# Performance work log

Measured on AMD Instinct MI355X. Metric: run time of the kernel, lower is better.

## Reference

```python
import jax, jax.numpy as jnp
import numpy as np

B, LQ, D, H, L, P, DFF = 16, 1024, 256, 8, 4, 4, 1024
SHAPES = ((64, 64), (32, 32), (16, 16), (8, 8))  # (H_l, W_l) per level
LV = sum(h * w for h, w in SHAPES)  # 5440
DH = D // H
EPS = 1e-5


def layer_norm(x, g, b):
    m = jnp.mean(x, -1, keepdims=True)
    v = jnp.mean((x - m) ** 2, -1, keepdims=True)
    return (x - m) * jax.lax.rsqrt(v + EPS) * g + b


def mha(q_in, k_in, v_in, w, b, ow, ob):
    # torch nn.MultiheadAttention with packed in_proj [3D, D]
    q = (q_in @ w[:D].T + b[:D]).reshape(B, LQ, H, DH)
    k = (k_in @ w[D:2 * D].T + b[D:2 * D]).reshape(B, LQ, H, DH)
    v = (v_in @ w[2 * D:].T + b[2 * D:]).reshape(B, LQ, H, DH)
    a = jax.nn.softmax(jnp.einsum('bqhd,bkhd->bhqk', q, k) * (1.0 / np.sqrt(DH)), -1)
    o = jnp.einsum('bhqk,bkhd->bqhd', a, v).reshape(B, LQ, D)
    return o @ ow.T + ob


def ms_deform_attn(q, ref, src, value_w, value_b, off_w, off_b, attw_w, attw_b, outp_w, outp_b):
    # value: [B, H, LV, DH]
    value = (src @ value_w.T + value_b).reshape(B, LV, H, DH).transpose(0, 2, 1, 3)
    off = (q @ off_w.T + off_b).reshape(B, LQ, H, L, P, 2)
    attw = jax.nn.softmax((q @ attw_w.T + attw_b).reshape(B, LQ, H, L * P), -1).reshape(B, LQ, H, L, P)
    # offset normalizer = (W_l, H_l) matching (x, y) order of reference points
    normalizer = jnp.array([[w, h] for h, w in SHAPES], jnp.float32)
    loc = ref[:, :, None, :, None, :] + off / normalizer[None, None, None, :, None, :]  # [B,LQ,H,L,P,2]
    out = jnp.zeros((B, LQ, H, DH), jnp.float32)
    start = 0
    for l, (hl, wl) in enumerate(SHAPES):
        v = value[:, :, start:start + hl * wl]  # [B,H,N_l,DH]
        start += hl * wl
        # grid_sample semantics, align_corners=False, padding zeros
        x = loc[:, :, :, l, :, 0] * wl - 0.5  # [B,LQ,H,P]
        y = loc[:, :, :, l, :, 1] * hl - 0.5
        x0 = jnp.floor(x); y0 = jnp.floor(y)
        lx = (x - x0).transpose(0, 2, 1, 3)[..., None]  # [B,H,LQ,P,1]
        ly = (y - y0).transpose(0, 2, 1, 3)[..., None]
        x0i = x0.astype(jnp.int32); y0i = y0.astype(jnp.int32)

        def gather(xi, yi):
            valid = ((xi >= 0) & (xi < wl) & (yi >= 0) & (yi < hl)).astype(jnp.float32)
            idx = jnp.clip(yi, 0, hl - 1) * wl + jnp.clip(xi, 0, wl - 1)  # [B,LQ,H,P]
            idx2 = idx.transpose(0, 2, 1, 3).reshape(B, H, LQ * P)
            g = jnp.take_along_axis(v, jnp.broadcast_to(idx2[..., None], (B, H, LQ * P, DH)), axis=2)
            return g.reshape(B, H, LQ, P, DH) * valid.transpose(0, 2, 1, 3)[..., None]

        g00 = gather(x0i, y0i); g01 = gather(x0i + 1, y0i)
        g10 = gather(x0i, y0i + 1); g11 = gather(x0i + 1, y0i + 1)
        sampled = (g00 * (1 - lx) * (1 - ly) + g01 * lx * (1 - ly)
                   + g10 * (1 - lx) * ly + g11 * lx * ly)  # [B,H,LQ,P,DH]
        out = out + jnp.einsum('bhqpd,bqhp->bqhd', sampled, attw[:, :, :, l])
    return out.reshape(B, LQ, D) @ outp_w.T + outp_b


def setup_inputs() -> dict:
    key = jax.random.key(0)
    ks = jax.random.split(key, 16)
    s = 0.02
    inp = {}
    inp['tgt'] = jax.random.normal(ks[0], (B, LQ, D), jnp.float32)
    inp['query_pos'] = jax.random.normal(ks[1], (B, LQ, D), jnp.float32)
    inp['reference_points'] = jax.random.uniform(ks[2], (B, LQ, L, 2), jnp.float32)
    inp['src'] = jax.random.normal(ks[3], (B, LV, D), jnp.float32)
    # self-attention (MHA)
    inp['in_proj_w'] = jax.random.normal(ks[4], (3 * D, D), jnp.float32) * s
    inp['in_proj_b'] = jnp.zeros((3 * D,), jnp.float32)
    inp['out_proj_w'] = jax.random.normal(ks[5], (D, D), jnp.float32) * s
    inp['out_proj_b'] = jnp.zeros((D,), jnp.float32)
    inp['norm2_g'] = jnp.ones((D,), jnp.float32); inp['norm2_b'] = jnp.zeros((D,), jnp.float32)
    # MSDeformAttn
    inp['value_w'] = jax.random.normal(ks[6], (D, D), jnp.float32) * s
    inp['value_b'] = jnp.zeros((D,), jnp.float32)
    inp['off_w'] = jax.random.normal(ks[7], (H * L * P * 2, D), jnp.float32) * s
    inp['off_b'] = jax.random.normal(ks[8], (H * L * P * 2,), jnp.float32) * 0.5
    inp['attw_w'] = jax.random.normal(ks[9], (H * L * P, D), jnp.float32) * s
    inp['attw_b'] = jnp.zeros((H * L * P,), jnp.float32)
    inp['outp_w'] = jax.random.normal(ks[10], (D, D), jnp.float32) * s
    inp['outp_b'] = jnp.zeros((D,), jnp.float32)
    inp['norm1_g'] = jnp.ones((D,), jnp.float32); inp['norm1_b'] = jnp.zeros((D,), jnp.float32)
    # FFN
    inp['lin1_w'] = jax.random.normal(ks[11], (DFF, D), jnp.float32) * s
    inp['lin1_b'] = jnp.zeros((DFF,), jnp.float32)
    inp['lin2_w'] = jax.random.normal(ks[12], (D, DFF), jnp.float32) * s
    inp['lin2_b'] = jnp.zeros((D,), jnp.float32)
    inp['norm3_g'] = jnp.ones((D,), jnp.float32); inp['norm3_b'] = jnp.zeros((D,), jnp.float32)
    inp['src_spatial_shapes'] = jnp.array(SHAPES, jnp.int32)
    inp['level_start_index'] = jnp.array(np.concatenate([[0], np.cumsum([h * w for h, w in SHAPES[:-1]])]), jnp.int32)
    return inp


def reference(tgt, query_pos, reference_points, src,
              in_proj_w, in_proj_b, out_proj_w, out_proj_b, norm2_g, norm2_b,
              value_w, value_b, off_w, off_b, attw_w, attw_b, outp_w, outp_b,
              norm1_g, norm1_b, lin1_w, lin1_b, lin2_w, lin2_b, norm3_g, norm3_b,
              src_spatial_shapes, level_start_index):
    # dropout=0 (eval mode)
    q = tgt + query_pos
    tgt2 = mha(q, q, tgt, in_proj_w, in_proj_b, out_proj_w, out_proj_b)
    tgt = layer_norm(tgt + tgt2, norm2_g, norm2_b)
    tgt2 = ms_deform_attn(tgt + query_pos, reference_points, src,
                          value_w, value_b, off_w, off_b, attw_w, attw_b, outp_w, outp_b)
    tgt = layer_norm(tgt + tgt2, norm1_g, norm1_b)
    t2 = jax.nn.relu(tgt @ lin1_w.T + lin1_b) @ lin2_w.T + lin2_b
    return layer_norm(tgt + t2, norm3_g, norm3_b)
```

## Files before the change

### kernel.cpp

```cpp
#include <hip/hip_runtime.h>
#include <math.h>

typedef short s16x8 __attribute__((ext_vector_type(8)));
typedef float f32x4 __attribute__((ext_vector_type(4)));
typedef unsigned short u16;
typedef unsigned short u16x4 __attribute__((ext_vector_type(4)));

constexpr int cB    = 16;
constexpr int cLQ   = 1024;
constexpr int cD    = 256;
constexpr int cH    = 8;
constexpr int cLVTOT= 5440;
constexpr int cNTOK = cB * cLQ;
constexpr int cNV   = cB * cLVTOT;

__device__ __forceinline__ u16 f2b(float f) {
    __bf16 h = (__bf16)f;
    u16 u;
    __builtin_memcpy(&u, &h, 2);
    return u;
}
__device__ __forceinline__ float bl(unsigned x) {
    return __uint_as_float(x << 16);
}
__device__ __forceinline__ void load16(const u16* g, u16* l) {
    __builtin_amdgcn_global_load_lds((const __attribute__((address_space(1))) void*)g,
                                     (__attribute__((address_space(3))) void*)l, 16, 0, 0);
}

__global__ __launch_bounds__(256) void cvt_kernel(const float4* __restrict__ in,
                                                  u16x4* __restrict__ out) {
    int i = blockIdx.x * 256 + threadIdx.x;
    float4 v = in[i];
    out[i] = (u16x4){ f2b(v.x), f2b(v.y), f2b(v.z), f2b(v.w) };
}

struct WArgs { const float4* src[8]; };
__global__ __launch_bounds__(256) void cvtw_kernel(WArgs a, u16x4* __restrict__ out) {
    int i = blockIdx.x * 256 + threadIdx.x;
    int s, off;
    if (i < 98304) {
        if (i < 65536) { if (i < 49152) { s = 0; off = i; } else { s = 1; off = i - 49152; } }
        else           { if (i < 81920) { s = 2; off = i - 65536; } else { s = 3; off = i - 81920; } }
    } else {
        if (i < 122880){ if (i < 106496){ s = 4; off = i - 98304; } else { s = 5; off = i - 106496; } }
        else           { if (i < 188416){ s = 6; off = i - 122880; } else { s = 7; off = i - 188416; } }
    }
    float4 v = a.src[s][off];
    out[i] = (u16x4){ f2b(v.x), f2b(v.y), f2b(v.z), f2b(v.w) };
}

__global__ __launch_bounds__(256) void prep_kernel(const float4* __restrict__ t,
                                                   const float4* __restrict__ q,
                                                   u16x4* __restrict__ tb,
                                                   u16x4* __restrict__ qb) {
    int i = blockIdx.x * 256 + threadIdx.x;
    float4 a = t[i], b = q[i];
    tb[i] = (u16x4){ f2b(a.x), f2b(a.y), f2b(a.z), f2b(a.w) };
    qb[i] = (u16x4){ f2b(a.x + b.x), f2b(a.y + b.y), f2b(a.z + b.z), f2b(a.w + b.w) };
}

__global__ __launch_bounds__(256) void gemm_qkv(const u16* __restrict__ A0,
                                                const u16* __restrict__ A1,
                                                const u16* __restrict__ Wt,
                                                const float* __restrict__ bias,
                                                u16* __restrict__ QKb,
                                                u16* __restrict__ Vtg) {
    __shared__ u16 As[2][128 * 32];
    __shared__ u16 Bs[2][128 * 32];
    const int K = 256;
    int tid = threadIdx.x;
    int bm = blockIdx.x * 128, bn = blockIdx.y * 128;
    const u16* A = (blockIdx.y < 4) ? A0 : A1;
    int w = tid >> 6, lane = tid & 63, quad = lane >> 4, l15 = lane & 15;
    int wm = (w & 1) * 64, wn = (w >> 1) * 64;
    int r0 = tid >> 2;
    int c0 = ((tid & 3) ^ ((tid >> 3) & 3)) * 8;
    const u16* ga0 = A  + (size_t)(bm + r0) * K + c0;
    const u16* ga1 = ga0 + (size_t)64 * K;
    const u16* gb0 = Wt + (size_t)(bn + r0) * K + c0;
    const u16* gb1 = gb0 + (size_t)64 * K;
    int lofs = (tid & 192) * 8;
    int abk = (quad ^ ((l15 >> 1) & 3)) * 8;
    f32x4 acc[16];
#pragma unroll
    for (int i = 0; i < 16; ++i) acc[i] = (f32x4){0.f, 0.f, 0.f, 0.f};
    load16(ga0, &As[0][lofs]);
    load16(ga1, &As[0][2048 + lofs]);
    load16(gb0, &Bs[0][lofs]);
    load16(gb1, &Bs[0][2048 + lofs]);
#pragma unroll 2
    for (int i = 0; i < 8; ++i) {
        int cur = i & 1, nxt = cur ^ 1;
        int k1 = (i + 1) << 5;
        if (i < 7) {
            load16(ga0 + k1, &As[nxt][lofs]);
            load16(ga1 + k1, &As[nxt][2048 + lofs]);
            load16(gb0 + k1, &Bs[nxt][lofs]);
            load16(gb1 + k1, &Bs[nxt][2048 + lofs]);
        }
        __syncthreads();
        s16x8 af[4], bf[4];
#pragma unroll
        for (int mt = 0; mt < 4; ++mt) af[mt] = *(const s16x8*)&As[cur][(wm + mt * 16 + l15) * 32 + abk];
#pragma unroll
        for (int nt = 0; nt < 4; ++nt) bf[nt] = *(const s16x8*)&Bs[cur][(wn + nt * 16 + l15) * 32 + abk];
#pragma unroll
        for (int mt = 0; mt < 4; ++mt)
#pragma unroll
            for (int nt = 0; nt < 4; ++nt)
                acc[mt * 4 + nt] = __builtin_amdgcn_mfma_f32_16x16x32_bf16(af[mt], bf[nt], acc[mt * 4 + nt], 0, 0, 0);
        __syncthreads();
    }
    float bs[4];
#pragma unroll
    for (int nt = 0; nt < 4; ++nt) bs[nt] = bias[bn + wn + nt * 16 + l15];
    if (bn < 512) {
#pragma unroll
        for (int mt = 0; mt < 4; ++mt) {
            int m = bm + wm + mt * 16 + quad * 4;
#pragma unroll
            for (int nt = 0; nt < 4; ++nt) {
                int n = bn + wn + nt * 16 + l15;
#pragma unroll
                for (int r = 0; r < 4; ++r)
                    QKb[(size_t)(m + r) * 512 + n] = f2b(acc[mt * 4 + nt][r] + bs[nt]);
            }
        }
    } else {
#pragma unroll
        for (int mt = 0; mt < 4; ++mt) {
            int m = bm + wm + mt * 16 + quad * 4;
            int b = m >> 10, t = m & 1023;
#pragma unroll
            for (int nt = 0; nt < 4; ++nt) {
                int nv = bn + wn + nt * 16 + l15 - 512;
                int h = nv >> 5, dh = nv & 31;
                u16x4 o;
#pragma unroll
                for (int r = 0; r < 4; ++r) o[r] = f2b(acc[mt * 4 + nt][r] + bs[nt]);
                *(u16x4*)(Vtg + (((size_t)(b * 8 + h) * 32 + dh) << 10) + t) = o;
            }
        }
    }
}

template <int RELU, int OUTBF>
__global__ __launch_bounds__(256) void gemm128(const u16* __restrict__ A,
                                               const u16* __restrict__ Wt,
                                               const float* __restrict__ bias,
                                               float* __restrict__ Cf,
                                               u16* __restrict__ Cb,
                                               int M, int N, int K) {
    __shared__ u16 As[2][128 * 32];
    __shared__ u16 Bs[2][128 * 32];
    int tid = threadIdx.x;
    int bm = blockIdx.x * 128, bn = blockIdx.y * 128;
    int w = tid >> 6, lane = tid & 63, quad = lane >> 4, l15 = lane & 15;
    int wm = (w & 1) * 64, wn = (w >> 1) * 64;
    int r0 = tid >> 2;
    int c0 = ((tid & 3) ^ ((tid >> 3) & 3)) * 8;
    const u16* ga0 = A  + (size_t)(bm + r0) * K + c0;
    const u16* ga1 = ga0 + (size_t)64 * K;
    const u16* gb0 = Wt + (size_t)(bn + r0) * K + c0;
    const u16* gb1 = gb0 + (size_t)64 * K;
    int lofs = (tid & 192) * 8;
    int abk = (quad ^ ((l15 >> 1) & 3)) * 8;
    f32x4 acc[16];
#pragma unroll
    for (int i = 0; i < 16; ++i) acc[i] = (f32x4){0.f, 0.f, 0.f, 0.f};
    load16(ga0, &As[0][lofs]);
    load16(ga1, &As[0][2048 + lofs]);
    load16(gb0, &Bs[0][lofs]);
    load16(gb1, &Bs[0][2048 + lofs]);
    int nk = K >> 5;
#pragma unroll 2
    for (int i = 0; i < nk; ++i) {
        int cur = i & 1, nxt = cur ^ 1;
        int k1 = (i + 1) << 5;
        if (i + 1 < nk) {
            load16(ga0 + k1, &As[nxt][lofs]);
            load16(ga1 + k1, &As[nxt][2048 + lofs]);
            load16(gb0 + k1, &Bs[nxt][lofs]);
            load16(gb1 + k1, &Bs[nxt][2048 + lofs]);
        }
        __syncthreads();
        s16x8 af[4], bf[4];
#pragma unroll
        for (int mt = 0; mt < 4; ++mt) af[mt] = *(const s16x8*)&As[cur][(wm + mt * 16 + l15) * 32 + abk];
#pragma unroll
        for (int nt = 0; nt < 4; ++nt) bf[nt] = *(const s16x8*)&Bs[cur][(wn + nt * 16 + l15) * 32 + abk];
#pragma unroll
        for (int mt = 0; mt < 4; ++mt)
#pragma unroll
            for (int nt = 0; nt < 4; ++nt)
                acc[mt * 4 + nt] = __builtin_amdgcn_mfma_f32_16x16x32_bf16(af[mt], bf[nt], acc[mt * 4 + nt], 0, 0, 0);
        __syncthreads();
    }
    float bs[4];
#pragma unroll
    for (int nt = 0; nt < 4; ++nt) bs[nt] = bias[bn + wn + nt * 16 + l15];
#pragma unroll
    for (int mt = 0; mt < 4; ++mt) {
        int m = bm + wm + mt * 16 + quad * 4;
#pragma unroll
        for (int nt = 0; nt < 4; ++nt) {
            int n = bn + wn + nt * 16 + l15;
#pragma unroll
            for (int r = 0; r < 4; ++r) {
                float v = acc[mt * 4 + nt][r] + bs[nt];
                if (RELU) v = fmaxf(v, 0.f);
                if (OUTBF) Cb[(size_t)(m + r) * N + n] = f2b(v);
                else       Cf[(size_t)(m + r) * N + n] = v;
            }
        }
    }
}

template <int RELU, int OUTBF>
__global__ __launch_bounds__(256) void gemm64(const u16* __restrict__ A,
                                              const u16* __restrict__ Wt,
                                              const float* __restrict__ bias,
                                              float* __restrict__ Cf,
                                              u16* __restrict__ Cb,
                                              int M, int N, int K) {
    __shared__ u16 As[2][64 * 32];
    __shared__ u16 Bs[2][128 * 32];
    int tid = threadIdx.x;
    int bm = blockIdx.x * 64, bn = blockIdx.y * 128;
    int w = tid >> 6, lane = tid & 63, quad = lane >> 4, l15 = lane & 15;
    int wn = w * 32;
    int r0 = tid >> 2;
    int c0 = ((tid & 3) ^ ((tid >> 3) & 3)) * 8;
    const u16* ga0 = A  + (size_t)(bm + r0) * K + c0;
    const u16* gb0 = Wt + (size_t)(bn + r0) * K + c0;
    const u16* gb1 = gb0 + (size_t)64 * K;
    int lofs = (tid & 192) * 8;
    int abk = (quad ^ ((l15 >> 1) & 3)) * 8;
    f32x4 acc[8];
#pragma unroll
    for (int i = 0; i < 8; ++i) acc[i] = (f32x4){0.f, 0.f, 0.f, 0.f};
    load16(ga0, &As[0][lofs]);
    load16(gb0, &Bs[0][lofs]);
    load16(gb1, &Bs[0][2048 + lofs]);
    int nk = K >> 5;
#pragma unroll 2
    for (int i = 0; i < nk; ++i) {
        int cur = i & 1, nxt = cur ^ 1;
        int k1 = (i + 1) << 5;
        if (i + 1 < nk) {
            load16(ga0 + k1, &As[nxt][lofs]);
            load16(gb0 + k1, &Bs[nxt][lofs]);
            load16(gb1 + k1, &Bs[nxt][2048 + lofs]);
        }
        __syncthreads();
        s16x8 af[4], bf[2];
#pragma unroll
        for (int mt = 0; mt < 4; ++mt) af[mt] = *(const s16x8*)&As[cur][(mt * 16 + l15) * 32 + abk];
#pragma unroll
        for (int nt = 0; nt < 2; ++nt) bf[nt] = *(const s16x8*)&Bs[cur][(wn + nt * 16 + l15) * 32 + abk];
#pragma unroll
        for (int mt = 0; mt < 4; ++mt)
#pragma unroll
            for (int nt = 0; nt < 2; ++nt)
                acc[mt * 2 + nt] = __builtin_amdgcn_mfma_f32_16x16x32_bf16(af[mt], bf[nt], acc[mt * 2 + nt], 0, 0, 0);
        __syncthreads();
    }
    float bs[2];
#pragma unroll
    for (int nt = 0; nt < 2; ++nt) bs[nt] = bias[bn + wn + nt * 16 + l15];
#pragma unroll
    for (int mt = 0; mt < 4; ++mt) {
        int m = bm + mt * 16 + quad * 4;
#pragma unroll
        for (int nt = 0; nt < 2; ++nt) {
            int n = bn + wn + nt * 16 + l15;
#pragma unroll
            for (int r = 0; r < 4; ++r) {
                float v = acc[mt * 2 + nt][r] + bs[nt];
                if (RELU) v = fmaxf(v, 0.f);
                if (OUTBF) Cb[(size_t)(m + r) * N + n] = f2b(v);
                else       Cf[(size_t)(m + r) * N + n] = v;
            }
        }
    }
}

__global__ __launch_bounds__(256) void attn_mfma(const u16* __restrict__ QK,
                                                 const u16* __restrict__ Vt,
                                                 u16* __restrict__ O) {
    __shared__ u16 Ks[64 * 40];
    __shared__ u16 Vs[32 * 72];
    __shared__ u16 Ps[4][16 * 72];
    int tid = threadIdx.x, w = tid >> 6, lane = tid & 63, quad = lane >> 4, l15 = lane & 15;
    int qt = blockIdx.x & 15, bh = blockIdx.x >> 4;
    int h = bh & 7, b = bh >> 3;
    int qbase = qt * 64 + w * 16;
    const float C = 0.25506734f;
    s16x8 qf = *(const s16x8*)(QK + (size_t)(b * cLQ + qbase + l15) * 512 + h * 32 + quad * 8);
    f32x4 o0 = {0.f,0.f,0.f,0.f}, o1 = {0.f,0.f,0.f,0.f};
    float lsum = 0.f;
    int skey = tid >> 2, sdh = (tid & 3) * 8;
    int vdh = tid >> 3, vkc = (tid & 7) * 8;
    size_t kgbase = (size_t)(b * cLQ) * 512 + 256 + h * 32;
    size_t vgbase = (size_t)bh * 32 * cLQ;
    s16x8 kreg = *(const s16x8*)(QK + kgbase + (size_t)skey * 512 + sdh);
    s16x8 vreg = *(const s16x8*)(Vt + vgbase + (size_t)vdh * cLQ + vkc);
    for (int kt = 0; kt < cLQ; kt += 64) {
        __syncthreads();
        *(s16x8*)&Ks[skey * 40 + sdh] = kreg;
        *(s16x8*)&Vs[vdh * 72 + vkc]  = vreg;
        if (kt + 64 < cLQ) {
            kreg = *(const s16x8*)(QK + kgbase + (size_t)(kt + 64 + skey) * 512 + sdh);
            vreg = *(const s16x8*)(Vt + vgbase + (size_t)vdh * cLQ + kt + 64 + vkc);
        }
        __syncthreads();
#pragma unroll
        for (int t = 0; t < 4; ++t) {
            s16x8 kf = *(const s16x8*)&Ks[(t * 16 + l15) * 40 + quad * 8];
            f32x4 z = {0.f,0.f,0.f,0.f};
            f32x4 sc = __builtin_amdgcn_mfma_f32_16x16x32_bf16(kf, qf, z, 0, 0, 0);
            u16x4 pb;
#pragma unroll
            for (int r = 0; r < 4; ++r) {
                float p = exp2f(sc[r] * C);
                lsum += p;
                pb[r] = f2b(p);
            }
            *(u16x4*)&Ps[w][l15 * 72 + t * 16 + quad * 4] = pb;
        }
#pragma unroll
        for (int ks = 0; ks < 2; ++ks) {
            s16x8 pa  = *(const s16x8*)&Ps[w][l15 * 72 + ks * 32 + quad * 8];
            s16x8 vb0 = *(const s16x8*)&Vs[l15 * 72 + ks * 32 + quad * 8];
            s16x8 vb1 = *(const s16x8*)&Vs[(l15 + 16) * 72 + ks * 32 + quad * 8];
            o0 = __builtin_amdgcn_mfma_f32_16x16x32_bf16(pa, vb0, o0, 0, 0, 0);
            o1 = __builtin_amdgcn_mfma_f32_16x16x32_bf16(pa, vb1, o1, 0, 0, 0);
        }
    }
    lsum += __shfl_xor(lsum, 16);
    lsum += __shfl_xor(lsum, 32);
#pragma unroll
    for (int r = 0; r < 4; ++r) {
        float inv = 1.0f / __shfl(lsum, quad * 4 + r);
        int q = qbase + quad * 4 + r;
        size_t ob = (size_t)(b * cLQ + q) * cD + h * 32;
        O[ob + l15]      = f2b(o0[r] * inv);
        O[ob + 16 + l15] = f2b(o1[r] * inv);
    }
}

template <int WB, int QP>
__global__ __launch_bounds__(256) void add_ln_kernel(const float* __restrict__ X,
                                                     const float* __restrict__ R,
                                                     const float* __restrict__ g,
                                                     const float* __restrict__ bt,
                                                     const float* __restrict__ qp,
                                                     float* __restrict__ out,
                                                     u16* __restrict__ outb) {
    int wave = threadIdx.x / 64;
    int lane = threadIdx.x % 64;
    int row = blockIdx.x * 4 + wave;
    const float* x = X + (size_t)row * cD;
    const float* r = R + (size_t)row * cD;
    float4 xv = *(const float4*)(x + lane * 4);
    float4 rv = *(const float4*)(r + lane * 4);
    float v0 = xv.x + rv.x, v1 = xv.y + rv.y, v2 = xv.z + rv.z, v3 = xv.w + rv.w;
    float s = v0 + v1 + v2 + v3;
    float s2 = v0 * v0 + v1 * v1 + v2 * v2 + v3 * v3;
#pragma unroll
    for (int off = 32; off > 0; off >>= 1) {
        s += __shfl_xor(s, off);
        s2 += __shfl_xor(s2, off);
    }
    float mean = s * (1.0f / 256.0f);
    float var = s2 * (1.0f / 256.0f) - mean * mean;
    float rstd = rsqrtf(var + 1e-5f);
    float4 gv = *(const float4*)(g + lane * 4);
    float4 bv = *(const float4*)(bt + lane * 4);
    float4 o;
    o.x = (v0 - mean) * rstd * gv.x + bv.x;
    o.y = (v1 - mean) * rstd * gv.y + bv.y;
    o.z = (v2 - mean) * rstd * gv.z + bv.z;
    o.w = (v3 - mean) * rstd * gv.w + bv.w;
    *(float4*)(out + (size_t)row * cD + lane * 4) = o;
    if (WB) {
        u16x4 ob = { f2b(o.x), f2b(o.y), f2b(o.z), f2b(o.w) };
        *(u16x4*)(outb + (size_t)row * cD + lane * 4) = ob;
    }
    if (QP) {
        float4 qv = *(const float4*)(qp + (size_t)row * cD + lane * 4);
        u16x4 ob = { f2b(o.x + qv.x), f2b(o.y + qv.y), f2b(o.z + qv.z), f2b(o.w + qv.w) };
        *(u16x4*)(outb + (size_t)row * cD + lane * 4) = ob;
    }
}

__global__ __launch_bounds__(256) void deform_kernel(const u16* __restrict__ value,
                                                     const float* __restrict__ oa,
                                                     const float* __restrict__ refp,
                                                     u16* __restrict__ out) {
    int t = blockIdx.x * 32 + (threadIdx.x >> 3);
    int dq = threadIdx.x & 7;
    int h = t & 7;
    int bq = t >> 3;
    int b = bq >> 10;
    const float* al = oa + (size_t)bq * 384 + 256 + h * 16;
    float wv[16];
    float mx = -1e30f;
#pragma unroll
    for (int i = 0; i < 16; ++i) { wv[i] = al[i]; mx = fmaxf(mx, wv[i]); }
    float sum = 0.f;
#pragma unroll
    for (int i = 0; i < 16; ++i) { wv[i] = __expf(wv[i] - mx); sum += wv[i]; }
    float inv = 1.f / sum;
    const float* off = oa + (size_t)bq * 384 + h * 32;
    const float* rp = refp + (size_t)bq * 8;
    const u16* vb = value + ((size_t)b * cLVTOT) * 256 + h * 32 + dq * 4;
    const int starts[4] = {0, 4096, 5120, 5376};
    const int dims[4] = {64, 32, 16, 8};
    float a0 = 0.f, a1 = 0.f, a2 = 0.f, a3 = 0.f;
#pragma unroll
    for (int l = 0; l < 4; ++l) {
        int hl = dims[l], wl = dims[l];
        float rx = rp[l * 2 + 0], ry = rp[l * 2 + 1];
#pragma unroll
        for (int p = 0; p < 4; ++p) {
            float ox = off[(l * 4 + p) * 2 + 0];
            float oy = off[(l * 4 + p) * 2 + 1];
            float x = rx * (float)wl + ox - 0.5f;
            float y = ry * (float)hl + oy - 0.5f;
            float x0f = floorf(x), y0f = floorf(y);
            float lx = x - x0f, ly = y - y0f;
            int x0 = (int)x0f, y0 = (int)y0f;
            float aw = wv[l * 4 + p] * inv;
            float cw[4] = {(1.f - lx) * (1.f - ly), lx * (1.f - ly),
                           (1.f - lx) * ly, lx * ly};
            int xs[4] = {x0, x0 + 1, x0, x0 + 1};
            int ys[4] = {y0, y0, y0 + 1, y0 + 1};
#pragma unroll
            for (int c = 0; c < 4; ++c) {
                int xi = xs[c], yi = ys[c];
                bool valid = (xi >= 0) && (xi < wl) && (yi >= 0) && (yi < hl);
                int xc = min(max(xi, 0), wl - 1);
                int yc = min(max(yi, 0), hl - 1);
                int idx = starts[l] + yc * wl + xc;
                float wgt = valid ? aw * cw[c] : 0.f;
                unsigned long long u = *(const unsigned long long*)(vb + (size_t)idx * 256);
                a0 += wgt * bl((unsigned)(u & 0xffffull));
                a1 += wgt * bl((unsigned)((u >> 16) & 0xffffull));
                a2 += wgt * bl((unsigned)((u >> 32) & 0xffffull));
                a3 += wgt * bl((unsigned)(u >> 48));
            }
        }
    }
    u16x4 o = { f2b(a0), f2b(a1), f2b(a2), f2b(a3) };
    *(u16x4*)(out + (size_t)bq * 256 + h * 32 + dq * 4) = o;
}

extern "C" void kernel_launch(void* const* d_in, const int* in_sizes, int n_in,
                              void* d_out, int out_size, void* d_ws, size_t ws_size,
                              hipStream_t stream) {
    const float* tgt        = (const float*)d_in[0];
    const float* query_pos  = (const float*)d_in[1];
    const float* refp       = (const float*)d_in[2];
    const float* src        = (const float*)d_in[3];
    const float* in_proj_w  = (const float*)d_in[4];
    const float* in_proj_b  = (const float*)d_in[5];
    const float* out_proj_w = (const float*)d_in[6];
    const float* out_proj_b = (const float*)d_in[7];
    const float* norm2_g    = (const float*)d_in[8];
    const float* norm2_b    = (const float*)d_in[9];
    const float* value_w    = (const float*)d_in[10];
    const float* value_b    = (const float*)d_in[11];
    const float* off_b      = (const float*)d_in[13];
    const float* attw_b     = (const float*)d_in[15];
    const float* outp_b     = (const float*)d_in[17];
    const float* norm1_g    = (const float*)d_in[18];
    const float* norm1_b    = (const float*)d_in[19];
    const float* lin1_b     = (const float*)d_in[21];
    const float* lin2_b     = (const float*)d_in[23];
    const float* norm3_g    = (const float*)d_in[24];
    const float* norm3_b    = (const float*)d_in[25];

    char* W = (char*)d_ws;
    const size_t S84 = 8388608;
    u16*   tgtb  = (u16*)(W + 0);
    u16*   q2b   = (u16*)(W + 0);
    u16*   qb    = (u16*)(W + 1 * S84);
    u16*   QKb   = (u16*)(W + 2 * S84);
    u16*   dtb   = (u16*)(W + 2 * S84);
    u16*   x2b   = (u16*)(W + 3 * S84);
    float* ffn2f = (float*)(W + 4 * S84);
    u16*   aob   = (u16*)(W + 5 * S84);
    float* oaf   = (float*)(W + 5 * S84);
    u16*   Vtg   = (u16*)(W + 6 * S84);
    float* t2f   = (float*)(W + 6 * S84);
    float* x1f   = (float*)(W + 8 * S84);
    float* x2f   = (float*)(W + 10 * S84);
    u16*   srcb  = (u16*)(W + 12 * S84);
    u16*   ffn1b = (u16*)(W + 12 * S84);
    u16*   valb  = (u16*)(W + 12 * S84 + 44564480);
    char*  wbase = W + 12 * S84 + 2 * 44564480;
    u16* wb_in   = (u16*)(wbase + 0);
    u16* wb_out  = (u16*)(wbase + 393216);
    u16* wb_val  = (u16*)(wbase + 524288);
    u16* wb_off  = (u16*)(wbase + 655360);
    u16* wb_outp = (u16*)(wbase + 851968);
    u16* wb_lin1 = (u16*)(wbase + 983040);
    u16* wb_lin2 = (u16*)(wbase + 1507328);
    float* biasoa= (float*)(wbase + 2031616);
    float* out = (float*)d_out;

    dim3 blk(256);

    hipMemcpyAsync(biasoa,       off_b,  256 * 4, hipMemcpyDeviceToDevice, stream);
    hipMemcpyAsync(biasoa + 256, attw_b, 128 * 4, hipMemcpyDeviceToDevice, stream);

    prep_kernel<<<dim3(4096), blk, 0, stream>>>((const float4*)tgt, (const float4*)query_pos,
                                                (u16x4*)tgtb, (u16x4*)qb);
    WArgs wa;
    wa.src[0] = (const float4*)in_proj_w;  wa.src[1] = (const float4*)out_proj_w;
    wa.src[2] = (const float4*)value_w;    wa.src[3] = (const float4*)d_in[12];
    wa.src[4] = (const float4*)d_in[14];   wa.src[5] = (const float4*)d_in[16];
    wa.src[6] = (const float4*)d_in[20];   wa.src[7] = (const float4*)d_in[22];
    cvtw_kernel<<<dim3(992), blk, 0, stream>>>(wa, (u16x4*)wb_in);
    cvt_kernel<<<dim3(21760), blk, 0, stream>>>((const float4*)src, (u16x4*)srcb);

    gemm_qkv<<<dim3(128, 6), blk, 0, stream>>>(qb, tgtb, wb_in, in_proj_b, QKb, Vtg);
    attn_mfma<<<dim3(cB * cH * 16), blk, 0, stream>>>(QKb, Vtg, aob);
    gemm64<0, 0><<<dim3(256, 2), blk, 0, stream>>>(aob, wb_out, out_proj_b, t2f, nullptr, cNTOK, 256, 256);
    add_ln_kernel<0, 1><<<dim3(4096), blk, 0, stream>>>(tgt, t2f, norm2_g, norm2_b, query_pos, x1f, q2b);

    gemm128<0, 1><<<dim3(680, 2), blk, 0, stream>>>(srcb, wb_val, value_b, nullptr, valb, cNV, 256, 256);
    gemm64<0, 0><<<dim3(256, 3), blk, 0, stream>>>(q2b, wb_off, biasoa, oaf, nullptr, cNTOK, 384, 256);
    deform_kernel<<<dim3(4096), blk, 0, stream>>>(valb, oaf, refp, dtb);
    gemm64<0, 0><<<dim3(256, 2), blk, 0, stream>>>(dtb, wb_outp, outp_b, t2f, nullptr, cNTOK, 256, 256);
    add_ln_kernel<1, 0><<<dim3(4096), blk, 0, stream>>>(x1f, t2f, norm1_g, norm1_b, nullptr, x2f, x2b);

    gemm128<1, 1><<<dim3(128, 8), blk, 0, stream>>>(x2b, wb_lin1, lin1_b, nullptr, ffn1b, cNTOK, 1024, 256);
    gemm64<0, 0><<<dim3(256, 2), blk, 0, stream>>>(ffn1b, wb_lin2, lin2_b, ffn2f, nullptr, cNTOK, 256, 1024);
    add_ln_kernel<0, 0><<<dim3(4096), blk, 0, stream>>>(x2f, ffn2f, norm3_g, norm3_b, nullptr, out, nullptr);
}
```

Before: 458.0 us.

## Stage GEMM tiles through registers, fuse prep kernels, fold softmax scale into Q

```diff
diff --git a/kernel.cpp b/kernel.cpp
--- a/kernel.cpp
+++ b/kernel.cpp
@@ -23,21 +23,38 @@
 __device__ __forceinline__ float bl(unsigned x) {
     return __uint_as_float(x << 16);
 }
-__device__ __forceinline__ void load16(const u16* g, u16* l) {
-    __builtin_amdgcn_global_load_lds((const __attribute__((address_space(1))) void*)g,
-                                     (__attribute__((address_space(3))) void*)l, 16, 0, 0);
-}
-
-__global__ __launch_bounds__(256) void cvt_kernel(const float4* __restrict__ in,
-                                                  u16x4* __restrict__ out) {
+
+__global__ __launch_bounds__(256) void prep_src_kernel(const float4* __restrict__ t,
+                                                       const float4* __restrict__ q,
+                                                       u16x4* __restrict__ tb,
+                                                       u16x4* __restrict__ qb,
+                                                       const float4* __restrict__ src,
+                                                       u16x4* __restrict__ srcb) {
+    int bid = blockIdx.x;
+    if (bid < 4096) {
+        int i = bid * 256 + threadIdx.x;
+        float4 a = t[i], b = q[i];
+        tb[i] = (u16x4){ f2b(a.x), f2b(a.y), f2b(a.z), f2b(a.w) };
+        qb[i] = (u16x4){ f2b(a.x + b.x), f2b(a.y + b.y), f2b(a.z + b.z), f2b(a.w + b.w) };
+    } else {
+        int i = (bid - 4096) * 256 + threadIdx.x;
+        float4 v = src[i];
+        srcb[i] = (u16x4){ f2b(v.x), f2b(v.y), f2b(v.z), f2b(v.w) };
+    }
+}
+
+struct WArgs { const float4* src[8]; };
+__global__ __launch_bounds__(256) void cvtw_kernel(WArgs a, u16x4* __restrict__ out,
+                                                   const float* __restrict__ off_b,
+                                                   const float* __restrict__ attw_b,
+                                                   float* __restrict__ biasoa) {
     int i = blockIdx.x * 256 + threadIdx.x;
-    float4 v = in[i];
-    out[i] = (u16x4){ f2b(v.x), f2b(v.y), f2b(v.z), f2b(v.w) };
-}
-
-struct WArgs { const float4* src[8]; };
-__global__ __launch_bounds__(256) void cvtw_kernel(WArgs a, u16x4* __restrict__ out) {
-    int i = blockIdx.x * 256 + threadIdx.x;
+    if (i >= 253952) {
+        int t = threadIdx.x;
+        biasoa[t] = off_b[t];
+        if (t < 128) biasoa[256 + t] = attw_b[t];
+        return;
+    }
     int s, off;
     if (i < 98304) {
         if (i < 65536) { if (i < 49152) { s = 0; off = i; } else { s = 1; off = i - 49152; } }
@@ -50,24 +67,14 @@
     out[i] = (u16x4){ f2b(v.x), f2b(v.y), f2b(v.z), f2b(v.w) };
 }
 
-__global__ __launch_bounds__(256) void prep_kernel(const float4* __restrict__ t,
-                                                   const float4* __restrict__ q,
-                                                   u16x4* __restrict__ tb,
-                                                   u16x4* __restrict__ qb) {
-    int i = blockIdx.x * 256 + threadIdx.x;
-    float4 a = t[i], b = q[i];
-    tb[i] = (u16x4){ f2b(a.x), f2b(a.y), f2b(a.z), f2b(a.w) };
-    qb[i] = (u16x4){ f2b(a.x + b.x), f2b(a.y + b.y), f2b(a.z + b.z), f2b(a.w + b.w) };
-}
-
 __global__ __launch_bounds__(256) void gemm_qkv(const u16* __restrict__ A0,
                                                 const u16* __restrict__ A1,
                                                 const u16* __restrict__ Wt,
                                                 const float* __restrict__ bias,
                                                 u16* __restrict__ QKb,
                                                 u16* __restrict__ Vtg) {
-    __shared__ u16 As[2][128 * 32];
-    __shared__ u16 Bs[2][128 * 32];
+    __shared__ u16 As[128 * 32];
+    __shared__ u16 Bs[128 * 32];
     const int K = 256;
     int tid = threadIdx.x;
     int bm = blockIdx.x * 128, bn = blockIdx.y * 128;
@@ -80,31 +87,29 @@
     const u16* ga1 = ga0 + (size_t)64 * K;
     const u16* gb0 = Wt + (size_t)(bn + r0) * K + c0;
     const u16* gb1 = gb0 + (size_t)64 * K;
-    int lofs = (tid & 192) * 8;
     int abk = (quad ^ ((l15 >> 1) & 3)) * 8;
     f32x4 acc[16];
 #pragma unroll
     for (int i = 0; i < 16; ++i) acc[i] = (f32x4){0.f, 0.f, 0.f, 0.f};
-    load16(ga0, &As[0][lofs]);
-    load16(ga1, &As[0][2048 + lofs]);
-    load16(gb0, &Bs[0][lofs]);
-    load16(gb1, &Bs[0][2048 + lofs]);
+    s16x8 ra0 = *(const s16x8*)ga0, ra1 = *(const s16x8*)ga1;
+    s16x8 rb0 = *(const s16x8*)gb0, rb1 = *(const s16x8*)gb1;
 #pragma unroll 2
     for (int i = 0; i < 8; ++i) {
-        int cur = i & 1, nxt = cur ^ 1;
-        int k1 = (i + 1) << 5;
+        *(s16x8*)&As[tid * 8]        = ra0;
+        *(s16x8*)&As[2048 + tid * 8] = ra1;
+        *(s16x8*)&Bs[tid * 8]        = rb0;
+        *(s16x8*)&Bs[2048 + tid * 8] = rb1;
+        __syncthreads();
         if (i < 7) {
-            load16(ga0 + k1, &As[nxt][lofs]);
-            load16(ga1 + k1, &As[nxt][2048 + lofs]);
-            load16(gb0 + k1, &Bs[nxt][lofs]);
-            load16(gb1 + k1, &Bs[nxt][2048 + lofs]);
-        }
-        __syncthreads();
+            int k1 = (i + 1) << 5;
+            ra0 = *(const s16x8*)(ga0 + k1); ra1 = *(const s16x8*)(ga1 + k1);
+            rb0 = *(const s16x8*)(gb0 + k1); rb1 = *(const s16x8*)(gb1 + k1);
+        }
         s16x8 af[4], bf[4];
 #pragma unroll
-        for (int mt = 0; mt < 4; ++mt) af[mt] = *(const s16x8*)&As[cur][(wm + mt * 16 + l15) * 32 + abk];
-#pragma unroll
-        for (int nt = 0; nt < 4; ++nt) bf[nt] = *(const s16x8*)&Bs[cur][(wn + nt * 16 + l15) * 32 + abk];
+        for (int mt = 0; mt < 4; ++mt) af[mt] = *(const s16x8*)&As[(wm + mt * 16 + l15) * 32 + abk];
+#pragma unroll
+        for (int nt = 0; nt < 4; ++nt) bf[nt] = *(const s16x8*)&Bs[(wn + nt * 16 + l15) * 32 + abk];
 #pragma unroll
         for (int mt = 0; mt < 4; ++mt)
 #pragma unroll
@@ -116,6 +121,7 @@
 #pragma unroll
     for (int nt = 0; nt < 4; ++nt) bs[nt] = bias[bn + wn + nt * 16 + l15];
     if (bn < 512) {
+        float qs = (bn + wn < 256) ? 0.25506734f : 1.0f;
 #pragma unroll
         for (int mt = 0; mt < 4; ++mt) {
             int m = bm + wm + mt * 16 + quad * 4;
@@ -124,7 +130,7 @@
                 int n = bn + wn + nt * 16 + l15;
 #pragma unroll
                 for (int r = 0; r < 4; ++r)
-                    QKb[(size_t)(m + r) * 512 + n] = f2b(acc[mt * 4 + nt][r] + bs[nt]);
+                    QKb[(size_t)(m + r) * 512 + n] = f2b((acc[mt * 4 + nt][r] + bs[nt]) * qs);
             }
         }
     } else {
@@ -152,8 +158,8 @@
                                                float* __restrict__ Cf,
                                                u16* __restrict__ Cb,
                                                int M, int N, int K) {
-    __shared__ u16 As[2][128 * 32];
-    __shared__ u16 Bs[2][128 * 32];
+    __shared__ u16 As[128 * 32];
+    __shared__ u16 Bs[128 * 32];
     int tid = threadIdx.x;
     int bm = blockIdx.x * 128, bn = blockIdx.y * 128;
     int w = tid >> 6, lane = tid & 63, quad = lane >> 4, l15 = lane & 15;
@@ -164,32 +170,30 @@
     const u16* ga1 = ga0 + (size_t)64 * K;
     const u16* gb0 = Wt + (size_t)(bn + r0) * K + c0;
     const u16* gb1 = gb0 + (size_t)64 * K;
-    int lofs = (tid & 192) * 8;
     int abk = (quad ^ ((l15 >> 1) & 3)) * 8;
     f32x4 acc[16];
 #pragma unroll
     for (int i = 0; i < 16; ++i) acc[i] = (f32x4){0.f, 0.f, 0.f, 0.f};
-    load16(ga0, &As[0][lofs]);
-    load16(ga1, &As[0][2048 + lofs]);
-    load16(gb0, &Bs[0][lofs]);
-    load16(gb1, &Bs[0][2048 + lofs]);
+    s16x8 ra0 = *(const s16x8*)ga0, ra1 = *(const s16x8*)ga1;
+    s16x8 rb0 = *(const s16x8*)gb0, rb1 = *(const s16x8*)gb1;
     int nk = K >> 5;
 #pragma unroll 2
     for (int i = 0; i < nk; ++i) {
-        int cur = i & 1, nxt = cur ^ 1;
-        int k1 = (i + 1) << 5;
+        *(s16x8*)&As[tid * 8]        = ra0;
+        *(s16x8*)&As[2048 + tid * 8] = ra1;
+        *(s16x8*)&Bs[tid * 8]        = rb0;
+        *(s16x8*)&Bs[2048 + tid * 8] = rb1;
+        __syncthreads();
         if (i + 1 < nk) {
-            load16(ga0 + k1, &As[nxt][lofs]);
-            load16(ga1 + k1, &As[nxt][2048 + lofs]);
-            load16(gb0 + k1, &Bs[nxt][lofs]);
-            load16(gb1 + k1, &Bs[nxt][2048 + lofs]);
-        }
-        __syncthreads();
+            int k1 = (i + 1) << 5;
+            ra0 = *(const s16x8*)(ga0 + k1); ra1 = *(const s16x8*)(ga1 + k1);
+            rb0 = *(const s16x8*)(gb0 + k1); rb1 = *(const s16x8*)(gb1 + k1);
+        }
         s16x8 af[4], bf[4];
 #pragma unroll
-        for (int mt = 0; mt < 4; ++mt) af[mt] = *(const s16x8*)&As[cur][(wm + mt * 16 + l15) * 32 + abk];
-#pragma unroll
-        for (int nt = 0; nt < 4; ++nt) bf[nt] = *(const s16x8*)&Bs[cur][(wn + nt * 16 + l15) * 32 + abk];
+        for (int mt = 0; mt < 4; ++mt) af[mt] = *(const s16x8*)&As[(wm + mt * 16 + l15) * 32 + abk];
+#pragma unroll
+        for (int nt = 0; nt < 4; ++nt) bf[nt] = *(const s16x8*)&Bs[(wn + nt * 16 + l15) * 32 + abk];
 #pragma unroll
         for (int mt = 0; mt < 4; ++mt)
 #pragma unroll
@@ -224,8 +228,8 @@
                                               float* __restrict__ Cf,
                                               u16* __restrict__ Cb,
                                               int M, int N, int K) {
-    __shared__ u16 As[2][64 * 32];
-    __shared__ u16 Bs[2][128 * 32];
+    __shared__ u16 As[64 * 32];
+    __shared__ u16 Bs[128 * 32];
     int tid = threadIdx.x;
     int bm = blockIdx.x * 64, bn = blockIdx.y * 128;
     int w = tid >> 6, lane = tid & 63, quad = lane >> 4, l15 = lane & 15;
@@ -235,30 +239,29 @@
     const u16* ga0 = A  + (size_t)(bm + r0) * K + c0;
     const u16* gb0 = Wt + (size_t)(bn + r0) * K + c0;
     const u16* gb1 = gb0 + (size_t)64 * K;
-    int lofs = (tid & 192) * 8;
     int abk = (quad ^ ((l15 >> 1) & 3)) * 8;
     f32x4 acc[8];
 #pragma unroll
     for (int i = 0; i < 8; ++i) acc[i] = (f32x4){0.f, 0.f, 0.f, 0.f};
-    load16(ga0, &As[0][lofs]);
-    load16(gb0, &Bs[0][lofs]);
-    load16(gb1, &Bs[0][2048 + lofs]);
+    s16x8 ra0 = *(const s16x8*)ga0;
+    s16x8 rb0 = *(const s16x8*)gb0, rb1 = *(const s16x8*)gb1;
     int nk = K >> 5;
 #pragma unroll 2
     for (int i = 0; i < nk; ++i) {
-        int cur = i & 1, nxt = cur ^ 1;
-        int k1 = (i + 1) << 5;
+        *(s16x8*)&As[tid * 8]        = ra0;
+        *(s16x8*)&Bs[tid * 8]        = rb0;
+        *(s16x8*)&Bs[2048 + tid * 8] = rb1;
+        __syncthreads();
         if (i + 1 < nk) {
-            load16(ga0 + k1, &As[nxt][lofs]);
-            load16(gb0 + k1, &Bs[nxt][lofs]);
-            load16(gb1 + k1, &Bs[nxt][2048 + lofs]);
-        }
-        __syncthreads();
+            int k1 = (i + 1) << 5;
+            ra0 = *(const s16x8*)(ga0 + k1);
+            rb0 = *(const s16x8*)(gb0 + k1); rb1 = *(const s16x8*)(gb1 + k1);
+        }
         s16x8 af[4], bf[2];
 #pragma unroll
-        for (int mt = 0; mt < 4; ++mt) af[mt] = *(const s16x8*)&As[cur][(mt * 16 + l15) * 32 + abk];
-#pragma unroll
-        for (int nt = 0; nt < 2; ++nt) bf[nt] = *(const s16x8*)&Bs[cur][(wn + nt * 16 + l15) * 32 + abk];
+        for (int mt = 0; mt < 4; ++mt) af[mt] = *(const s16x8*)&As[(mt * 16 + l15) * 32 + abk];
+#pragma unroll
+        for (int nt = 0; nt < 2; ++nt) bf[nt] = *(const s16x8*)&Bs[(wn + nt * 16 + l15) * 32 + abk];
 #pragma unroll
         for (int mt = 0; mt < 4; ++mt)
 #pragma unroll
@@ -296,7 +299,6 @@
     int qt = blockIdx.x & 15, bh = blockIdx.x >> 4;
     int h = bh & 7, b = bh >> 3;
     int qbase = qt * 64 + w * 16;
-    const float C = 0.25506734f;
     s16x8 qf = *(const s16x8*)(QK + (size_t)(b * cLQ + qbase + l15) * 512 + h * 32 + quad * 8);
     f32x4 o0 = {0.f,0.f,0.f,0.f}, o1 = {0.f,0.f,0.f,0.f};
     float lsum = 0.f;
@@ -323,7 +325,7 @@
             u16x4 pb;
 #pragma unroll
             for (int r = 0; r < 4; ++r) {
-                float p = exp2f(sc[r] * C);
+                float p = exp2f(sc[r]);
                 lsum += p;
                 pb[r] = f2b(p);
             }
@@ -466,11 +468,9 @@
     const float* src        = (const float*)d_in[3];
     const float* in_proj_w  = (const float*)d_in[4];
     const float* in_proj_b  = (const float*)d_in[5];
-    const float* out_proj_w = (const float*)d_in[6];
     const float* out_proj_b = (const float*)d_in[7];
     const float* norm2_g    = (const float*)d_in[8];
     const float* norm2_b    = (const float*)d_in[9];
-    const float* value_w    = (const float*)d_in[10];
     const float* value_b    = (const float*)d_in[11];
     const float* off_b      = (const float*)d_in[13];
     const float* attw_b     = (const float*)d_in[15];
@@ -513,18 +513,15 @@
 
     dim3 blk(256);
 
-    hipMemcpyAsync(biasoa,       off_b,  256 * 4, hipMemcpyDeviceToDevice, stream);
-    hipMemcpyAsync(biasoa + 256, attw_b, 128 * 4, hipMemcpyDeviceToDevice, stream);
-
-    prep_kernel<<<dim3(4096), blk, 0, stream>>>((const float4*)tgt, (const float4*)query_pos,
-                                                (u16x4*)tgtb, (u16x4*)qb);
+    prep_src_kernel<<<dim3(25856), blk, 0, stream>>>((const float4*)tgt, (const float4*)query_pos,
+                                                     (u16x4*)tgtb, (u16x4*)qb,
+                                                     (const float4*)src, (u16x4*)srcb);
     WArgs wa;
-    wa.src[0] = (const float4*)in_proj_w;  wa.src[1] = (const float4*)out_proj_w;
-    wa.src[2] = (const float4*)value_w;    wa.src[3] = (const float4*)d_in[12];
+    wa.src[0] = (const float4*)in_proj_w;  wa.src[1] = (const float4*)d_in[6];
+    wa.src[2] = (const float4*)d_in[10];   wa.src[3] = (const float4*)d_in[12];
     wa.src[4] = (const float4*)d_in[14];   wa.src[5] = (const float4*)d_in[16];
     wa.src[6] = (const float4*)d_in[20];   wa.src[7] = (const float4*)d_in[22];
-    cvtw_kernel<<<dim3(992), blk, 0, stream>>>(wa, (u16x4*)wb_in);
-    cvt_kernel<<<dim3(21760), blk, 0, stream>>>((const float4*)src, (u16x4*)srcb);
+    cvtw_kernel<<<dim3(993), blk, 0, stream>>>(wa, (u16x4*)wb_in, off_b, attw_b, biasoa);
 
     gemm_qkv<<<dim3(128, 6), blk, 0, stream>>>(qb, tgtb, wb_in, in_proj_b, QKb, Vtg);
     attn_mfma<<<dim3(cB * cH * 16), blk, 0, stream>>>(QKb, Vtg, aob);
```

Result: faster. 436.7 us (-4.7%).
